# Performance work log

Measured on AMD Instinct MI355X. Metric: run time of the kernel, lower is better.

Reference implementation:

```python
import jax, jax.numpy as jnp
import numpy as np

B, T, H, K = 16, 2048, 512, 15
FIRE_TH = 1.0
SMOOTH = 1.0
NOISE_TH = 0.0
LN_EPS = 1e-5


def setup_inputs() -> dict:
    key = jax.random.key(0)
    ks = jax.random.split(key, 8)
    s = lambda n: 1.0 / np.sqrt(n)
    return {
        "x": jax.random.normal(ks[0], (B, T, H), jnp.float32),
        "x_lens": jax.random.randint(ks[1], (B,), T // 2, T + 1),
        "pw1_w": jax.random.normal(ks[2], (2 * H, H), jnp.float32) * s(H),
        "pw1_b": jnp.zeros((2 * H,), jnp.float32),
        "dw_w": jax.random.normal(ks[3], (H, K), jnp.float32) * s(K),
        "dw_b": jnp.zeros((H,), jnp.float32),
        "ln_g": jnp.ones((H,), jnp.float32),
        "ln_b": jnp.zeros((H,), jnp.float32),
        "pw2_w": jax.random.normal(ks[4], (H, H), jnp.float32) * s(H),
        "pw2_b": jnp.zeros((H,), jnp.float32),
        "lin_w": jax.random.normal(ks[5], (H,), jnp.float32) * s(H),
        "lin_b": jnp.zeros((), jnp.float32),
    }


def _layer_norm(x, g, b):
    m = x.mean(-1, keepdims=True)
    v = ((x - m) ** 2).mean(-1, keepdims=True)
    return (x - m) * jax.lax.rsqrt(v + LN_EPS) * g + b


def _swish(x):
    return x * jax.nn.sigmoid(x)


def _conv_module(x, pw1_w, pw1_b, dw_w, dw_b, ln_g, ln_b, pw2_w, pw2_b):
    # wenet ConvolutionModule (causal, layer_norm): pw-conv -> GLU -> causal depthwise -> LN -> swish -> pw-conv
    h = jnp.einsum('bth,oh->bto', x, pw1_w) + pw1_b          # (B,T,2H)
    h = h[..., :H] * jax.nn.sigmoid(h[..., H:])              # GLU over channel halves
    hp = jnp.pad(h, ((0, 0), (K - 1, 0), (0, 0)))            # causal left pad
    rhs = dw_w.T[:, None, :]                                 # (K, 1, H) depthwise kernel
    h = jax.lax.conv_general_dilated(
        hp, rhs, window_strides=(1,), padding='VALID',
        dimension_numbers=('NWC', 'WIO', 'NWC'),
        feature_group_count=H) + dw_b                        # (B,T,H)
    h = _swish(_layer_norm(h, ln_g, ln_b))
    return jnp.einsum('bth,oh->bto', h, pw2_w) + pw2_b


def _cif_scan(x, alphas):
    # sequential integrate-and-fire over time, batched over B
    def step(carry, inp):
        integrate, frame = carry
        alpha, xt = inp                                       # (B,), (B,H)
        dist = FIRE_TH - integrate
        integrate = integrate + alpha
        fire = integrate >= FIRE_TH
        cur = jnp.where(fire, dist, alpha)
        remain = alpha - cur
        frame_acc = frame + cur[:, None] * xt
        new_frame = jnp.where(fire[:, None], remain[:, None] * xt, frame_acc)
        new_int = jnp.where(fire, integrate - FIRE_TH, integrate)
        return (new_int, new_frame), (integrate, frame_acc)
    init = (jnp.zeros((B,), x.dtype), jnp.zeros((B, H), x.dtype))
    _, (fires, frames) = jax.lax.scan(step, init, (alphas.T, x.transpose(1, 0, 2)))
    return fires.T, frames.transpose(1, 0, 2)                 # (B,T), (B,T,H)


def _gather_fired(fires, frames):
    # ragged gather of fired frames into a fixed (B,T,H) padded buffer
    mask = fires >= FIRE_TH                                   # (B,T)
    dest = jnp.where(mask, jnp.cumsum(mask, axis=1) - 1, T)   # dump non-fired to slot T
    out = jnp.zeros((B, T + 1, H), frames.dtype)
    out = out.at[jnp.arange(B)[:, None], dest].set(frames)
    fired = out[:, :T]
    return fired, jnp.flip(fired, axis=-1)                    # torch.flip(dims=[1]) flips hidden dim


def reference(x, x_lens, pw1_w, pw1_b, dw_w, dw_b, ln_g, ln_b, pw2_w, pw2_b, lin_w, lin_b):
    mask = (jnp.arange(T)[None, :] < x_lens[:, None]).astype(x.dtype)   # (B,T)
    hidden = _conv_module(x, pw1_w, pw1_b, dw_w, dw_b, ln_g, ln_b, pw2_w, pw2_b)
    logits = jnp.einsum('bth,h->bt', hidden, lin_w) + lin_b
    alphas = jax.nn.relu(jax.nn.sigmoid(logits) * SMOOTH - NOISE_TH) * mask
    predicted_token_nums = alphas.sum(-1)
    fires, frames = _cif_scan(x, alphas)
    fired_frames, r_fired_frames = _gather_fired(fires, frames)
    return fired_frames, predicted_token_nums, r_fired_frames
```

## Files before the change

### kernel.cpp

```cpp
#include <hip/hip_runtime.h>
#include <math.h>

#define B_ 16
#define T_ 2048
#define H_ 512
#define K_ 15
#define M_ (B_*T_)

typedef __attribute__((ext_vector_type(8))) short short8;
typedef __attribute__((ext_vector_type(4))) float f32x4;

__device__ __forceinline__ unsigned short f2bf(float f) {
  union { float f; unsigned u; } v; v.f = f;
  unsigned r = v.u + 0x7FFFu + ((v.u >> 16) & 1u);
  return (unsigned short)(r >> 16);
}
__device__ __forceinline__ float bf2f(unsigned short b) {
  union { float f; unsigned u; } v; v.u = ((unsigned)b) << 16;
  return v.f;
}

__device__ __forceinline__ void async_load16(const void* g, void* l) {
  __builtin_amdgcn_global_load_lds((const __attribute__((address_space(1))) void*)g,
                                   (__attribute__((address_space(3))) void*)l, 16, 0, 0);
}

__global__ void convx_k(const float* __restrict__ x, unsigned short* __restrict__ hi,
                        unsigned short* __restrict__ lo, int n4) {
  int i = blockIdx.x * blockDim.x + threadIdx.x;
  int stride = gridDim.x * blockDim.x;
  for (; i < n4; i += stride) {
    float4 v = ((const float4*)x)[i];
    ushort4 h, l;
    h.x = f2bf(v.x); l.x = f2bf(v.x - bf2f(h.x));
    h.y = f2bf(v.y); l.y = f2bf(v.y - bf2f(h.y));
    h.z = f2bf(v.z); l.z = f2bf(v.z - bf2f(h.z));
    h.w = f2bf(v.w); l.w = f2bf(v.w - bf2f(h.w));
    ((ushort4*)hi)[i] = h;
    ((ushort4*)lo)[i] = l;
  }
}

__global__ __launch_bounds__(256) void weff_k(const float* __restrict__ pw2_w,
    const float* __restrict__ pw2_b, const float* __restrict__ lin_w,
    const float* __restrict__ lin_b, float* __restrict__ weff) {
  __shared__ float red[256];
  if (blockIdx.x < 8) {
    int h = blockIdx.x * 64 + (threadIdx.x & 63);
    int og = threadIdx.x >> 6;
    float acc = 0.f;
    for (int o = og * 128; o < og * 128 + 128; ++o) acc += pw2_w[o * H_ + h] * lin_w[o];
    red[threadIdx.x] = acc;
    __syncthreads();
    if (threadIdx.x < 64)
      weff[h] = red[threadIdx.x] + red[threadIdx.x + 64] + red[threadIdx.x + 128] + red[threadIdx.x + 192];
  } else {
    int i = threadIdx.x;
    red[i] = pw2_b[i] * lin_w[i] + pw2_b[i + 256] * lin_w[i + 256];
    __syncthreads();
    for (int s = 128; s > 0; s >>= 1) {
      if (i < s) red[i] += red[i + s];
      __syncthreads();
    }
    if (i == 0) weff[H_] = red[0] + lin_b[0];
  }
}

__global__ __launch_bounds__(256) void gemm_mfma_k(
    const unsigned short* __restrict__ Ahi, const unsigned short* __restrict__ Alo,
    const unsigned short* __restrict__ Whi, const unsigned short* __restrict__ Wlo,
    const float* __restrict__ bias, float* __restrict__ g) {
  __shared__ short Ah[128 * 32];
  __shared__ short Al[128 * 32];
  __shared__ short Bh[128 * 32];
  __shared__ short Bl[128 * 32];
  const int tid = threadIdx.x;
  const int m0 = blockIdx.x * 128;
  const int n0 = blockIdx.y * 64;
  const int w = tid >> 6, lane = tid & 63;
  const int wr = w >> 1, wc = w & 1;

  f32x4 acc[4][4];
#pragma unroll
  for (int mt = 0; mt < 4; ++mt)
#pragma unroll
    for (int nt = 0; nt < 4; ++nt) acc[mt][nt] = (f32x4){0.f, 0.f, 0.f, 0.f};

  int offA[2], offB[2], ldsb[2];
#pragma unroll
  for (int j = 0; j < 2; ++j) {
    int L = j * 256 + tid;
    int r = L >> 2;
    int csrc = (L & 3) ^ ((r >> 1) & 3);
    offA[j] = (m0 + r) * 512 + csrc * 8;
    int wrow = (r < 64) ? (n0 + r) : (n0 + 448 + r);
    offB[j] = wrow * 512 + csrc * 8;
    ldsb[j] = __builtin_amdgcn_readfirstlane((j * 256 + w * 64) * 16);
  }

  const int q = lane >> 4;
  int aAddr[4], bAddr[4];
#pragma unroll
  for (int mt = 0; mt < 4; ++mt) {
    int rA = wr * 64 + mt * 16 + (lane & 15);
    aAddr[mt] = rA * 64 + (q ^ ((rA >> 1) & 3)) * 16;
  }
#pragma unroll
  for (int nt = 0; nt < 4; ++nt) {
    int rB = (nt >> 1) * 64 + wc * 32 + (nt & 1) * 16 + (lane & 15);
    bAddr[nt] = rB * 64 + (q ^ ((rB >> 1) & 3)) * 16;
  }

#pragma unroll 1
  for (int kk = 0; kk < 16; ++kk) {
    const int k0 = kk * 32;
    __syncthreads();
#pragma unroll
    for (int j = 0; j < 2; ++j) {
      async_load16(Ahi + offA[j] + k0, (char*)Ah + ldsb[j]);
      async_load16(Alo + offA[j] + k0, (char*)Al + ldsb[j]);
      async_load16(Whi + offB[j] + k0, (char*)Bh + ldsb[j]);
      async_load16(Wlo + offB[j] + k0, (char*)Bl + ldsb[j]);
    }
    __syncthreads();
    short8 ah[4], al[4], bh[4], bl[4];
#pragma unroll
    for (int mt = 0; mt < 4; ++mt) {
      ah[mt] = *(const short8*)((const char*)Ah + aAddr[mt]);
      al[mt] = *(const short8*)((const char*)Al + aAddr[mt]);
    }
#pragma unroll
    for (int nt = 0; nt < 4; ++nt) {
      bh[nt] = *(const short8*)((const char*)Bh + bAddr[nt]);
      bl[nt] = *(const short8*)((const char*)Bl + bAddr[nt]);
    }
#pragma unroll
    for (int mt = 0; mt < 4; ++mt)
#pragma unroll
      for (int nt = 0; nt < 4; ++nt) {
        acc[mt][nt] = __builtin_amdgcn_mfma_f32_16x16x32_bf16(ah[mt], bh[nt], acc[mt][nt], 0, 0, 0);
        acc[mt][nt] = __builtin_amdgcn_mfma_f32_16x16x32_bf16(al[mt], bh[nt], acc[mt][nt], 0, 0, 0);
        acc[mt][nt] = __builtin_amdgcn_mfma_f32_16x16x32_bf16(ah[mt], bl[nt], acc[mt][nt], 0, 0, 0);
      }
  }

  const int col = lane & 15, rq = lane >> 4;
#pragma unroll
  for (int mt = 0; mt < 4; ++mt) {
#pragma unroll
    for (int ntp = 0; ntp < 2; ++ntp) {
      int gcol = n0 + wc * 32 + ntp * 16 + col;
      float ba = bias[gcol];
      float bg = bias[512 + gcol];
#pragma unroll
      for (int r = 0; r < 4; ++r) {
        int m = m0 + wr * 64 + mt * 16 + rq * 4 + r;
        float a = acc[mt][ntp][r] + ba;
        float gt = acc[mt][2 + ntp][r] + bg;
        g[(size_t)m * 512 + gcol] = a / (1.f + expf(-gt));
      }
    }
  }
}

__global__ __launch_bounds__(512) void conv_ln_k(const float* __restrict__ g,
    const float* __restrict__ dw_w, const float* __restrict__ dw_b,
    const float* __restrict__ ln_g, const float* __restrict__ ln_b,
    const float* __restrict__ weff, const int* __restrict__ x_lens,
    float* __restrict__ aT) {
  __shared__ float wlds[H_ * K_];
  __shared__ float tbuf[16][512];
  __shared__ float mvs[16], rss[16];
  const int tid = threadIdx.x;
  const int c = tid;
  const int t0 = blockIdx.x * 64;
  const int b = blockIdx.y;

  for (int i = tid; i < H_ * K_; i += 512) wlds[i] = dw_w[i];
  const int xlen = x_lens[b];
  const float* gb = g + ((size_t)b * T_) * H_ + c;

  float gwin[30];
#pragma unroll
  for (int i = 0; i < 30; ++i) {
    int t = t0 - 14 + i;
    gwin[i] = (t >= 0) ? gb[(size_t)t * H_] : 0.f;
  }
  __syncthreads();
  float wreg[15];
#pragma unroll
  for (int k = 0; k < 15; ++k) wreg[k] = wlds[c * 15 + k];
  const float dwb = dw_b[c], lg = ln_g[c], lb = ln_b[c], we = weff[c];
  const float beff = weff[H_];
  const int tt = tid >> 5, p = tid & 31;

#pragma unroll 1
  for (int qc = 0; qc < 4; ++qc) {
    float h2[16];
#pragma unroll
    for (int j = 0; j < 16; ++j) {
      float s = dwb;
#pragma unroll
      for (int k = 0; k < 15; ++k) s += gwin[j + k] * wreg[k];
      h2[j] = s;
      tbuf[j][c] = s;
    }
    __syncthreads();
    float s1 = 0.f, s2 = 0.f;
#pragma unroll
    for (int k = 0; k < 16; ++k) {
      float v = tbuf[tt][k * 32 + p];
      s1 += v; s2 += v * v;
    }
#pragma unroll
    for (int off = 16; off > 0; off >>= 1) {
      s1 += __shfl_down(s1, off, 32);
      s2 += __shfl_down(s2, off, 32);
    }
    if (p == 0) {
      float m = s1 * (1.f / 512.f);
      float v = s2 * (1.f / 512.f) - m * m;
      mvs[tt] = m;
      rss[tt] = rsqrtf(v + 1e-5f);
    }
    __syncthreads();
#pragma unroll
    for (int j = 0; j < 16; ++j) {
      float y = (h2[j] - mvs[j]) * rss[j] * lg + lb;
      float sw = y / (1.f + expf(-y));
      tbuf[j][c] = sw * we;
    }
    __syncthreads();
    float s = 0.f;
#pragma unroll
    for (int k = 0; k < 16; ++k) s += tbuf[tt][k * 32 + p];
#pragma unroll
    for (int off = 16; off > 0; off >>= 1) s += __shfl_down(s, off, 32);
    if (p == 0) {
      float logit = s + beff;
      float a = 1.f / (1.f + expf(-logit));
      int t = t0 + qc * 16 + tt;
      if (t >= xlen) a = 0.f;
      aT[t * B_ + b] = a;
    }
    if (qc < 3) {
#pragma unroll
      for (int i = 0; i < 14; ++i) gwin[i] = gwin[i + 16];
#pragma unroll
      for (int i = 0; i < 16; ++i)
        gwin[14 + i] = gb[(size_t)(t0 + qc * 16 + 16 + i) * H_];
    }
    __syncthreads();
  }
}

__global__ __launch_bounds__(64) void cif_p1_k(const float* __restrict__ aT,
                                               float* __restrict__ chk) {
  const int b = threadIdx.x;
  if (b >= B_) return;
  const float* ar = aT + b;
  float integ = 0.f;
  float bufA[32], bufB[32];
#pragma unroll
  for (int j = 0; j < 32; ++j) bufA[j] = ar[j * B_];
#pragma unroll 1
  for (int s = 0; s < 64; s += 2) {
#pragma unroll
    for (int j = 0; j < 32; ++j) bufB[j] = ar[((s + 1) * 32 + j) * B_];
    chk[s * B_ + b] = integ;
#pragma unroll
    for (int j = 0; j < 32; ++j) {
      float ni = integ + bufA[j];
      integ = ni - floorf(ni);
    }
    if (s + 2 < 64) {
#pragma unroll
      for (int j = 0; j < 32; ++j) bufA[j] = ar[((s + 2) * 32 + j) * B_];
    }
    chk[(s + 1) * B_ + b] = integ;
#pragma unroll
    for (int j = 0; j < 32; ++j) {
      float ni = integ + bufB[j];
      integ = ni - floorf(ni);
    }
  }
}

__global__ __launch_bounds__(64) void cif_p2_k(const float* __restrict__ aT,
    const float* __restrict__ chk, float* __restrict__ wdT, float* __restrict__ wrT,
    int* __restrict__ fire_pos, int* __restrict__ nfires, float* __restrict__ tok) {
  const int b = blockIdx.x;
  const int seg = threadIdx.x;
  const int t0 = seg * 32;
  float integ = chk[seg * B_ + b];
  float a[32];
#pragma unroll
  for (int j = 0; j < 32; ++j) a[j] = aT[(t0 + j) * B_ + b];
  unsigned fmask = 0u;
  float ssum = 0.f;
#pragma unroll
  for (int j = 0; j < 32; ++j) {
    float al = a[j];
    float dist = 1.0f - integ;
    float ni = integ + al;
    bool fire = ni >= 1.0f;
    float cur = fire ? dist : al;
    wdT[(t0 + j) * B_ + b] = cur;
    wrT[(t0 + j) * B_ + b] = al - cur;
    if (fire) fmask |= (1u << j);
    integ = ni - floorf(ni);
    ssum += al;
  }
  const int cnt = __popc(fmask);
  int incl = cnt;
#pragma unroll
  for (int off = 1; off < 64; off <<= 1) {
    int v = __shfl_up(incl, off, 64);
    if (seg >= off) incl += v;
  }
  int idx = incl - cnt;
  unsigned m = fmask;
  while (m) {
    int j = __ffs(m) - 1;
    m &= m - 1;
    fire_pos[b * T_ + idx++] = t0 + j;
  }
  if (seg == 63) nfires[b] = incl;
#pragma unroll
  for (int off = 32; off > 0; off >>= 1) ssum += __shfl_down(ssum, off, 64);
  if (seg == 0) tok[b] = ssum;
}

__global__ __launch_bounds__(128) void frames_k(const float* __restrict__ x,
    const float* __restrict__ aT, const float* __restrict__ wdT,
    const float* __restrict__ wrT, const int* __restrict__ fire_pos,
    const int* __restrict__ nfires, float* __restrict__ out0, float* __restrict__ out2) {
  const int b = blockIdx.y;
  const int j = blockIdx.x;
  const int h = threadIdx.x << 2;
  const size_t ob = ((size_t)b * T_ + j) * H_;
  if (j >= nfires[b]) {
    float4 z = make_float4(0.f, 0.f, 0.f, 0.f);
    *(float4*)(out0 + ob + h) = z;
    *(float4*)(out2 + ob + h) = z;
    return;
  }
  const int te = fire_pos[b * T_ + j];
  const int ts = (j > 0) ? fire_pos[b * T_ + j - 1] : -1;
  const float* xb = x + ((size_t)b * T_) * H_;
  float4 acc = make_float4(0.f, 0.f, 0.f, 0.f);
  if (j > 0) {
    float w = wrT[ts * B_ + b];
    float4 xv = *(const float4*)(xb + (size_t)ts * H_ + h);
    acc.x = w * xv.x; acc.y = w * xv.y; acc.z = w * xv.z; acc.w = w * xv.w;
  }
  for (int t = ts + 1; t < te; ++t) {
    float w = aT[t * B_ + b];
    float4 xv = *(const float4*)(xb + (size_t)t * H_ + h);
    acc.x += w * xv.x; acc.y += w * xv.y; acc.z += w * xv.z; acc.w += w * xv.w;
  }
  {
    float w = wdT[te * B_ + b];
    float4 xv = *(const float4*)(xb + (size_t)te * H_ + h);
    acc.x += w * xv.x; acc.y += w * xv.y; acc.z += w * xv.z; acc.w += w * xv.w;
  }
  *(float4*)(out0 + ob + h) = acc;
  float4 racc = make_float4(acc.w, acc.z, acc.y, acc.x);
  *(float4*)(out2 + ob + (H_ - 4 - h)) = racc;
}

extern "C" void kernel_launch(void* const* d_in, const int* in_sizes, int n_in,
                              void* d_out, int out_size, void* d_ws, size_t ws_size,
                              hipStream_t stream) {
  const float* x     = (const float*)d_in[0];
  const int*   xlens = (const int*)d_in[1];
  const float* pw1_w = (const float*)d_in[2];
  const float* pw1_b = (const float*)d_in[3];
  const float* dw_w  = (const float*)d_in[4];
  const float* dw_b  = (const float*)d_in[5];
  const float* ln_g  = (const float*)d_in[6];
  const float* ln_b  = (const float*)d_in[7];
  const float* pw2_w = (const float*)d_in[8];
  const float* pw2_b = (const float*)d_in[9];
  const float* lin_w = (const float*)d_in[10];
  const float* lin_b = (const float*)d_in[11];

  float* out0 = (float*)d_out;
  float* tok  = out0 + (size_t)B_ * T_ * H_;
  float* out2 = tok + B_;

  char* ws = (char*)d_ws;
  float* g             = (float*)ws;
  unsigned short* Ahi  = (unsigned short*)(ws + (size_t)M_ * H_ * 4);
  unsigned short* Alo  = Ahi + (size_t)M_ * H_;
  unsigned short* Whi  = Alo + (size_t)M_ * H_;
  unsigned short* Wlo  = Whi + (size_t)2 * H_ * H_;
  float* aT       = (float*)(Wlo + (size_t)2 * H_ * H_);
  float* wdT      = aT + B_ * T_;
  float* wrT      = wdT + B_ * T_;
  int*   fire_pos = (int*)(wrT + B_ * T_);
  int*   nfires   = fire_pos + B_ * T_;
  float* weff     = (float*)(nfires + 64);
  float* chk      = weff + 1024;

  convx_k<<<2048, 256, 0, stream>>>(x, Ahi, Alo, M_ * H_ / 4);
  convx_k<<<256, 256, 0, stream>>>(pw1_w, Whi, Wlo, 2 * H_ * H_ / 4);
  weff_k<<<9, 256, 0, stream>>>(pw2_w, pw2_b, lin_w, lin_b, weff);
  gemm_mfma_k<<<dim3(256, 8), 256, 0, stream>>>(Ahi, Alo, Whi, Wlo, pw1_b, g);
  conv_ln_k<<<dim3(32, 16), 512, 0, stream>>>(g, dw_w, dw_b, ln_g, ln_b, weff, xlens, aT);
  cif_p1_k<<<1, 64, 0, stream>>>(aT, chk);
  cif_p2_k<<<16, 64, 0, stream>>>(aT, chk, wdT, wrT, fire_pos, nfires, tok);
  frames_k<<<dim3(2048, 16), 128, 0, stream>>>(x, aT, wdT, wrT, fire_pos, nfires, out0, out2);
}
```

Before: 452.1 us.

## Double-buffer LDS tiles in MFMA GEMM to overlap global loads with compute

Doubles the four shared-memory tiles and prefetches the first K-slice before the loop. Each iteration then issues async global-to-LDS loads for the next slice while running MFMAs on the current one, with only one barrier per iteration instead of two. The aim is to hide global memory latency behind the split-bf16 MFMA work. In exchange, LDS per block doubles to 64KB, which can reduce how many blocks fit on a CU, and correctness depends on the barrier also waiting for the async copies.

```diff
diff --git a/kernel.cpp b/kernel.cpp
--- a/kernel.cpp
+++ b/kernel.cpp
@@ -70,10 +70,10 @@
     const unsigned short* __restrict__ Ahi, const unsigned short* __restrict__ Alo,
     const unsigned short* __restrict__ Whi, const unsigned short* __restrict__ Wlo,
     const float* __restrict__ bias, float* __restrict__ g) {
-  __shared__ short Ah[128 * 32];
-  __shared__ short Al[128 * 32];
-  __shared__ short Bh[128 * 32];
-  __shared__ short Bl[128 * 32];
+  __shared__ short Ah[2][128 * 32];
+  __shared__ short Al[2][128 * 32];
+  __shared__ short Bh[2][128 * 32];
+  __shared__ short Bl[2][128 * 32];
   const int tid = threadIdx.x;
   const int m0 = blockIdx.x * 128;
   const int n0 = blockIdx.y * 64;
@@ -111,29 +111,44 @@
     bAddr[nt] = rB * 64 + (q ^ ((rB >> 1) & 3)) * 16;
   }
 
-#pragma unroll 1
+#pragma unroll
+  for (int j = 0; j < 2; ++j) {
+    async_load16(Ahi + offA[j], (char*)Ah[0] + ldsb[j]);
+    async_load16(Alo + offA[j], (char*)Al[0] + ldsb[j]);
+    async_load16(Whi + offB[j], (char*)Bh[0] + ldsb[j]);
+    async_load16(Wlo + offB[j], (char*)Bl[0] + ldsb[j]);
+  }
+
+#pragma unroll 2
   for (int kk = 0; kk < 16; ++kk) {
-    const int k0 = kk * 32;
-    __syncthreads();
-#pragma unroll
-    for (int j = 0; j < 2; ++j) {
-      async_load16(Ahi + offA[j] + k0, (char*)Ah + ldsb[j]);
-      async_load16(Alo + offA[j] + k0, (char*)Al + ldsb[j]);
-      async_load16(Whi + offB[j] + k0, (char*)Bh + ldsb[j]);
-      async_load16(Wlo + offB[j] + k0, (char*)Bl + ldsb[j]);
-    }
-    __syncthreads();
+    const int cur = kk & 1;
+    const int nxt = cur ^ 1;
+    __syncthreads();
+
     short8 ah[4], al[4], bh[4], bl[4];
 #pragma unroll
     for (int mt = 0; mt < 4; ++mt) {
-      ah[mt] = *(const short8*)((const char*)Ah + aAddr[mt]);
-      al[mt] = *(const short8*)((const char*)Al + aAddr[mt]);
+      ah[mt] = *(const short8*)((const char*)Ah[cur] + aAddr[mt]);
+      al[mt] = *(const short8*)((const char*)Al[cur] + aAddr[mt]);
     }
 #pragma unroll
     for (int nt = 0; nt < 4; ++nt) {
-      bh[nt] = *(const short8*)((const char*)Bh + bAddr[nt]);
-      bl[nt] = *(const short8*)((const char*)Bl + bAddr[nt]);
-    }
+      bh[nt] = *(const short8*)((const char*)Bh[cur] + bAddr[nt]);
+      bl[nt] = *(const short8*)((const char*)Bl[cur] + bAddr[nt]);
+    }
+
+    if (kk < 15) {
+      const int k0 = (kk + 1) * 32;
+#pragma unroll
+      for (int j = 0; j < 2; ++j) {
+        async_load16(Ahi + offA[j] + k0, (char*)Ah[nxt] + ldsb[j]);
+        async_load16(Alo + offA[j] + k0, (char*)Al[nxt] + ldsb[j]);
+        async_load16(Whi + offB[j] + k0, (char*)Bh[nxt] + ldsb[j]);
+        async_load16(Wlo + offB[j] + k0, (char*)Bl[nxt] + ldsb[j]);
+      }
+    }
+    __builtin_amdgcn_sched_barrier(0);
+
 #pragma unroll
     for (int mt = 0; mt < 4; ++mt)
 #pragma unroll
```

Result: no change. 452.7 us (+0.1%).
